# Kernel tuning notes

Hardware: AMD Instinct MI355X
Metric: run time of the kernel (lower is better)

Reference implementation:

```python
import jax, jax.numpy as jnp
import numpy as np

PERIOD = 24
TREND_WINDOW = 24
HALF = TREND_WINDOW // 2          # 12
DROP = (TREND_WINDOW - 1) // 2    # 11 rows dropped off the batch axis (as in original)


def setup_inputs() -> dict:
    key = jax.random.key(0)
    x = jax.random.normal(key, (4096, 2048), dtype=jnp.float32)
    return {"x": x}


def _trend(x):
    # Centered moving average with boundary-clipped (variable-size) windows,
    # vectorized via an exclusive cumulative sum.  x: (B, T)
    B, T = x.shape
    cs = jnp.concatenate([jnp.zeros((B, 1), x.dtype), jnp.cumsum(x, axis=1)], axis=1)  # (B, T+1)
    i = jnp.arange(T)
    start = jnp.clip(i - HALF, 0, T)           # max(0, i - half_window)
    end = jnp.clip(i + HALF + 1, 0, T)         # min(T, i + half_window + 1)
    sums = cs[:, end] - cs[:, start]           # (B, T)
    counts = (end - start).astype(x.dtype)     # (T,)
    return sums / counts


def _seasonal(x):
    # Phase-wise mean: seasonal[b, t] = mean_{t' : t' % PERIOD == t % PERIOD} x[b, t']
    B, T = x.shape
    phase = jnp.arange(T) % PERIOD                                    # (T,)
    sums = jax.ops.segment_sum(x.T, phase, num_segments=PERIOD)      # (P, B)
    counts = jax.ops.segment_sum(jnp.ones((T,), x.dtype), phase, num_segments=PERIOD)  # (P,)
    means = sums / counts[:, None]                                    # (P, B)
    return means[phase].T                                             # (B, T)


def reference(x):
    trend = _trend(x)
    detrended = x - trend                 # additive method
    seasonal = _seasonal(detrended)
    residual = x - trend - seasonal
    out = jnp.stack([trend, seasonal, residual], axis=2)  # (B, T, 3)
    # drop_na: original slices along the batch axis
    return out[DROP:, :, :]
```

## Files before the change

kernel.cpp:

```cpp
#include <hip/hip_runtime.h>

#define TT 2048
#define BB 4096
#define DROP_ROWS 11
#define PERIOD 24
#define BLOCK 256
#define HALF 12

__global__ __launch_bounds__(BLOCK) void seasonal_decomp_kernel(
    const float* __restrict__ x, float* __restrict__ out) {
  __shared__ float sx[TT];
  __shared__ float sd[TT];
  __shared__ float pp[PERIOD][8];
  __shared__ float pmean[PERIOD];

  const int row = blockIdx.x + DROP_ROWS;

  {
    const float4* rx = (const float4*)(x + (size_t)row * TT);
    float4* s4 = (float4*)sx;
    #pragma unroll
    for (int i = 0; i < TT / 4 / BLOCK; ++i) {
      s4[threadIdx.x + i * BLOCK] = rx[threadIdx.x + i * BLOCK];
    }
  }
  __syncthreads();

  float tr[TT / BLOCK];
  #pragma unroll
  for (int i = 0; i < TT / BLOCK; ++i) {
    int t = threadIdx.x + i * BLOCK;
    int s = t - HALF; if (s < 0) s = 0;
    int e = t + HALF + 1; if (e > TT) e = TT;
    float sum = 0.f;
    for (int k = s; k < e; ++k) sum += sx[k];
    tr[i] = sum / (float)(e - s);
    sd[t] = sx[t] - tr[i];
  }
  __syncthreads();

  if (threadIdx.x < PERIOD * 8) {
    int p = threadIdx.x >> 3;
    int j = threadIdx.x & 7;
    int cnt = (p < 8) ? 86 : 85;
    float s = 0.f;
    for (int m = j; m < cnt; m += 8) s += sd[p + PERIOD * m];
    pp[p][j] = s;
  }
  __syncthreads();
  if (threadIdx.x < PERIOD) {
    float s = 0.f;
    #pragma unroll
    for (int j = 0; j < 8; ++j) s += pp[threadIdx.x][j];
    pmean[threadIdx.x] = s / ((threadIdx.x < 8) ? 86.f : 85.f);
  }
  __syncthreads();

  float* orow = out + (size_t)blockIdx.x * TT * 3;
  #pragma unroll
  for (int i = 0; i < TT / BLOCK; ++i) {
    int t = threadIdx.x + i * BLOCK;
    float sea = pmean[t % PERIOD];
    float res = sd[t] - sea;
    float3 v = make_float3(tr[i], sea, res);
    *(float3*)(orow + (size_t)t * 3) = v;
  }
}

extern "C" void kernel_launch(void* const* d_in, const int* in_sizes, int n_in,
                              void* d_out, int out_size, void* d_ws, size_t ws_size,
                              hipStream_t stream) {
  const float* x = (const float*)d_in[0];
  float* out = (float*)d_out;
  seasonal_decomp_kernel<<<BB - DROP_ROWS, BLOCK, 0, stream>>>(x, out);
}
```

Before: 33.58 us.

## Use wave-scan prefix sums for trend and stage output through LDS for float4 stores

Replaces the per-element 25-tap loop over shared memory with a block-wide prefix sum (wave shuffles plus per-wave totals), so each window sum becomes a difference of two cumulative values. The interleaved (trend, seasonal, residual) output is first written to a 6144-float LDS buffer and then copied out with coalesced float4 stores instead of strided float3 stores. This cuts LDS reads and improves global write coalescing. In exchange it uses more shared memory, which may lower occupancy, and float cumsum differencing can lose some precision.

```diff
diff --git a/kernel.cpp b/kernel.cpp
--- a/kernel.cpp
+++ b/kernel.cpp
@@ -6,65 +6,100 @@
 #define PERIOD 24
 #define BLOCK 256
 #define HALF 12
+#define WAVES (BLOCK / 64)
 
 __global__ __launch_bounds__(BLOCK) void seasonal_decomp_kernel(
     const float* __restrict__ x, float* __restrict__ out) {
-  __shared__ float sx[TT];
-  __shared__ float sd[TT];
+  __shared__ float buf[6144];
+  __shared__ float wt0[WAVES], wt1[WAVES];
   __shared__ float pp[PERIOD][8];
   __shared__ float pmean[PERIOD];
+  float* const sd = buf;
+  float* const cs = buf + 2048;
+  float* const sout = buf;
 
+  const int tid = threadIdx.x;
+  const int lane = tid & 63;
+  const int wave = tid >> 6;
   const int row = blockIdx.x + DROP_ROWS;
 
-  {
-    const float4* rx = (const float4*)(x + (size_t)row * TT);
-    float4* s4 = (float4*)sx;
-    #pragma unroll
-    for (int i = 0; i < TT / 4 / BLOCK; ++i) {
-      s4[threadIdx.x + i * BLOCK] = rx[threadIdx.x + i * BLOCK];
-    }
+  const float4* rx = (const float4*)(x + (size_t)row * TT);
+  float4 v0 = rx[tid];
+  float4 v1 = rx[tid + 256];
+
+  float s0 = v0.x + v0.y + v0.z + v0.w;
+  float s1 = v1.x + v1.y + v1.z + v1.w;
+  float i0 = s0, i1 = s1;
+  #pragma unroll
+  for (int off = 1; off < 64; off <<= 1) {
+    float t0 = __shfl_up(i0, off, 64);
+    float t1 = __shfl_up(i1, off, 64);
+    if (lane >= off) { i0 += t0; i1 += t1; }
+  }
+  if (lane == 63) { wt0[wave] = i0; wt1[wave] = i1; }
+  __syncthreads();
+  float W0 = 0.f, W1 = 0.f, H = 0.f;
+  #pragma unroll
+  for (int w = 0; w < WAVES; ++w) {
+    float a = wt0[w], b = wt1[w];
+    H += a;
+    if (w < wave) { W0 += a; W1 += b; }
+  }
+  const float P0 = W0 + (i0 - s0);
+  const float P1 = H + W1 + (i1 - s1);
+
+  float4 c0, c1;
+  c0.x = P0; c0.y = P0 + v0.x; c0.z = c0.y + v0.y; c0.w = c0.z + v0.z;
+  c1.x = P1; c1.y = P1 + v1.x; c1.z = c1.y + v1.y; c1.w = c1.z + v1.z;
+  ((float4*)cs)[tid] = c0;
+  ((float4*)cs)[tid + 256] = c1;
+  if (tid == 255) cs[TT] = P1 + s1;
+  __syncthreads();
+
+  float tr[8], sdr[8];
+  #pragma unroll
+  for (int j = 0; j < 8; ++j) {
+    int t = tid + 256 * j;
+    int s = t - HALF; if (s < 0) s = 0;
+    int e = t + HALF + 1; if (e > TT) e = TT;
+    float wsum = cs[e] - cs[s];
+    float xt = cs[t + 1] - cs[t];
+    tr[j] = wsum / (float)(e - s);
+    sdr[j] = xt - tr[j];
+    sd[t] = sdr[j];
   }
   __syncthreads();
 
-  float tr[TT / BLOCK];
-  #pragma unroll
-  for (int i = 0; i < TT / BLOCK; ++i) {
-    int t = threadIdx.x + i * BLOCK;
-    int s = t - HALF; if (s < 0) s = 0;
-    int e = t + HALF + 1; if (e > TT) e = TT;
-    float sum = 0.f;
-    for (int k = s; k < e; ++k) sum += sx[k];
-    tr[i] = sum / (float)(e - s);
-    sd[t] = sx[t] - tr[i];
-  }
-  __syncthreads();
-
-  if (threadIdx.x < PERIOD * 8) {
-    int p = threadIdx.x >> 3;
-    int j = threadIdx.x & 7;
+  if (tid < PERIOD * 8) {
+    int p = tid >> 3;
+    int j = tid & 7;
     int cnt = (p < 8) ? 86 : 85;
     float s = 0.f;
     for (int m = j; m < cnt; m += 8) s += sd[p + PERIOD * m];
     pp[p][j] = s;
   }
   __syncthreads();
-  if (threadIdx.x < PERIOD) {
+  if (tid < PERIOD) {
     float s = 0.f;
     #pragma unroll
-    for (int j = 0; j < 8; ++j) s += pp[threadIdx.x][j];
-    pmean[threadIdx.x] = s / ((threadIdx.x < 8) ? 86.f : 85.f);
+    for (int j = 0; j < 8; ++j) s += pp[tid][j];
+    pmean[tid] = s / ((tid < 8) ? 86.f : 85.f);
   }
   __syncthreads();
 
-  float* orow = out + (size_t)blockIdx.x * TT * 3;
   #pragma unroll
-  for (int i = 0; i < TT / BLOCK; ++i) {
-    int t = threadIdx.x + i * BLOCK;
+  for (int j = 0; j < 8; ++j) {
+    int t = tid + 256 * j;
     float sea = pmean[t % PERIOD];
-    float res = sd[t] - sea;
-    float3 v = make_float3(tr[i], sea, res);
-    *(float3*)(orow + (size_t)t * 3) = v;
+    sout[3 * t]     = tr[j];
+    sout[3 * t + 1] = sea;
+    sout[3 * t + 2] = sdr[j] - sea;
   }
+  __syncthreads();
+  float4* orow = (float4*)(out + (size_t)blockIdx.x * (TT * 3));
+  const float4* so4 = (const float4*)sout;
+  #pragma unroll
+  for (int j = 0; j < 6; ++j) orow[tid + 256 * j] = so4[tid + 256 * j];
 }
 
 extern "C" void kernel_launch(void* const* d_in, const int* in_sizes, int n_in,
```

New measurement: 27.36 us. 1.23x faster.
